# Performance work log

Hardware: AMD Instinct MI355X
Metric: run time of the kernel (lower is better)

The kernel has to match this reference:

```python
import jax, jax.numpy as jnp
import numpy as np

MOL_SIZE = 64      # points per molecule (all molecules equal-size -> block-diagonal attn)
NUM_HEADS = 8
CUTOFF = 8.0
NUM_RBF = 32
LN_EPS = 1e-5


def setup_inputs() -> dict:
    key = jax.random.key(0)
    ks = jax.random.split(key, 6)
    B, K, hidden = 1024, MOL_SIZE, 512
    H = NUM_HEADS
    N = B * K
    h = jax.random.normal(ks[0], (N, hidden), jnp.float32)
    pos = jax.random.normal(ks[1], (N, 3), jnp.float32) * 3.0  # spread so dists hit RBF centers
    batch = jnp.repeat(jnp.arange(B, dtype=jnp.int32), K)
    s = lambda fin: 1.0 / np.sqrt(fin)
    centers = jnp.linspace(0.0, CUTOFF, NUM_RBF).astype(jnp.float32)  # RBFEncoder buffer
    w_rbf = jax.random.normal(ks[2], (NUM_RBF, H), jnp.float32) * s(NUM_RBF)
    b_rbf = jnp.zeros((H,), jnp.float32)
    w_qkv = jax.random.normal(ks[3], (hidden, 3 * hidden), jnp.float32) * s(hidden)
    b_qkv = jnp.zeros((3 * hidden,), jnp.float32)
    w_out = jax.random.normal(ks[4], (hidden, hidden), jnp.float32) * s(hidden)
    b_out = jnp.zeros((hidden,), jnp.float32)
    gamma = jnp.ones((hidden,), jnp.float32)
    beta = jnp.zeros((hidden,), jnp.float32)
    return {"h": h, "pos": pos, "batch": batch, "centers": centers,
            "w_rbf": w_rbf, "b_rbf": b_rbf, "w_qkv": w_qkv, "b_qkv": b_qkv,
            "w_out": w_out, "b_out": b_out, "gamma": gamma, "beta": beta}


def reference(h, pos, batch, centers, w_rbf, b_rbf, w_qkv, b_qkv, w_out, b_out, gamma, beta):
    N, hidden = h.shape
    K = MOL_SIZE
    B = N // K
    H = NUM_HEADS
    D = hidden // H
    width = (CUTOFF / NUM_RBF) ** 2
    scale = D ** -0.5

    # equal-size contiguous molecules -> reshape equals per-molecule loop
    hb = h.reshape(B, K, hidden)
    pb = pos.reshape(B, K, 3)

    qkv = hb @ w_qkv + b_qkv                      # [B,K,3*hidden]
    q, k, v = jnp.split(qkv, 3, axis=-1)
    q = q.reshape(B, K, H, D)
    k = k.reshape(B, K, H, D)
    v = v.reshape(B, K, H, D)

    diff = pb[:, :, None, :] - pb[:, None, :, :]  # [B,K,K,3]
    dist = jnp.sqrt(jnp.maximum(jnp.sum(diff * diff, axis=-1), 1e-12))  # torch.cdist
    rbf = jnp.exp(-((dist[..., None] - centers) ** 2) / width)          # [B,K,K,R]
    bias = jnp.transpose(rbf @ w_rbf + b_rbf, (0, 3, 1, 2))             # [B,H,K,K]

    attn = jnp.einsum('bkhd,bjhd->bhkj', q, k) * scale + bias
    attn = jax.nn.softmax(attn, axis=-1)
    agg = jnp.einsum('bhkj,bjhd->bkhd', attn, v).reshape(B, K, hidden)
    out = agg @ w_out + b_out

    y = hb + out
    mu = jnp.mean(y, axis=-1, keepdims=True)
    var = jnp.var(y, axis=-1, keepdims=True)
    y = (y - mu) / jnp.sqrt(var + LN_EPS) * gamma + beta
    return y.reshape(N, hidden)
```

## Files before the change

### kernel.cpp

```cpp
#include <hip/hip_runtime.h>
#include <hip/hip_bf16.h>


#define HID 512
#define TBL 1024
#define DMAX 12.0f

typedef __attribute__((ext_vector_type(4))) float f32x4;
typedef __attribute__((ext_vector_type(8))) short bhalf8;

__device__ __forceinline__ short f2bf(float f) {
    union { float f; unsigned u; } x; x.f = f;
    unsigned u = x.u;
    unsigned r = (u + 0x7FFFu + ((u >> 16) & 1u)) >> 16;
    return (short)r;
}

__global__ __launch_bounds__(256) void k_prep_w(const float* __restrict__ w_qkv,
                                                const float* __restrict__ w_out,
                                                short* __restrict__ wqT,
                                                short* __restrict__ woT) {
    __shared__ short tile[64][68];
    const int t = threadIdx.x;
    int bt = blockIdx.x;
    const float* src; short* dst; int sld, tk, tc;
    if (bt < 192) { src = w_qkv; dst = wqT; sld = 1536; tk = bt & 7; tc = bt >> 3; }
    else { int b2 = bt - 192; src = w_out; dst = woT; sld = 512; tk = b2 & 7; tc = b2 >> 3; }
#pragma unroll
    for (int p = 0; p < 4; ++p) {
        int s = t + 256 * p;
        int r = s >> 4, sg = s & 15;
        const float4 v = *(const float4*)(src + (tk * 64 + r) * sld + tc * 64 + sg * 4);
        tile[r][sg * 4 + 0] = f2bf(v.x);
        tile[r][sg * 4 + 1] = f2bf(v.y);
        tile[r][sg * 4 + 2] = f2bf(v.z);
        tile[r][sg * 4 + 3] = f2bf(v.w);
    }
    __syncthreads();
#pragma unroll
    for (int p = 0; p < 16; ++p) {
        int o = t + 256 * p;
        int c = o >> 6, k = o & 63;
        dst[(tc * 64 + c) * 512 + tk * 64 + k] = tile[k][c];
    }
}

__global__ __launch_bounds__(256) void k_prep_tbl(const float* __restrict__ centers,
                                                  const float* __restrict__ w_rbf,
                                                  const float* __restrict__ b_rbf,
                                                  float* __restrict__ tbl) {
    int idx = blockIdx.x * 256 + threadIdx.x;
    int hh = idx >> 10, i = idx & (TBL - 1);
    float d = (float)i * (DMAX / (float)(TBL - 1));
    float s = b_rbf[hh];
    const float invw = 1.0f / 0.0625f;
#pragma unroll 4
    for (int r = 0; r < 32; ++r) {
        float tt = d - centers[r];
        s += w_rbf[r * 8 + hh] * expf(-(tt * tt) * invw);
    }
    tbl[idx] = s;
}

__global__ __launch_bounds__(512) void k_qkv(const float* __restrict__ h,
                                             const float* __restrict__ b_qkv,
                                             const short* __restrict__ wqT,
                                             short* __restrict__ qkvb,
                                             int molbase) {
    __shared__ __align__(16) short As[2][128 * 40];
    __shared__ __align__(16) short Bs[2][256 * 40];
    const int t = threadIdx.x;
    const int lane = t & 63, wave = t >> 6;
    const int l16 = lane & 15, g = lane >> 4;
    const int wrow = wave >> 2, wcol = wave & 3;
    const int R0 = molbase * 64 + blockIdx.x * 128;
    const int C0 = blockIdx.y * 256;

    f32x4 acc[4][4];
#pragma unroll
    for (int i = 0; i < 4; ++i)
#pragma unroll
        for (int j = 0; j < 4; ++j) acc[i][j] = (f32x4){0.f, 0.f, 0.f, 0.f};

    const int arow = t >> 2, aseg = t & 3;
    const float* hsrc = h + (size_t)(R0 + arow) * HID + aseg * 8;
    const int bcol = t >> 2, bseg = t & 3;
    const short* bsrc0 = wqT + (size_t)(C0 + bcol) * HID + bseg * 8;
    const short* bsrc1 = wqT + (size_t)(C0 + bcol + 128) * HID + bseg * 8;

    int4 pA, pB0, pB1;
#define QLOADA(kc) {                                                             \
        float4 a0 = *(const float4*)(hsrc + (kc) * 32);                          \
        float4 a1 = *(const float4*)(hsrc + (kc) * 32 + 4);                      \
        short s8[8];                                                             \
        s8[0] = f2bf(a0.x); s8[1] = f2bf(a0.y); s8[2] = f2bf(a0.z); s8[3] = f2bf(a0.w); \
        s8[4] = f2bf(a1.x); s8[5] = f2bf(a1.y); s8[6] = f2bf(a1.z); s8[7] = f2bf(a1.w); \
        pA = *(int4*)s8; }
#define QLOADB(kc) {                                                             \
        pB0 = *(const int4*)(bsrc0 + (kc) * 32);                                 \
        pB1 = *(const int4*)(bsrc1 + (kc) * 32); }
#define QSTAGE(buf) {                                                            \
        *(int4*)(&As[buf][arow * 40 + aseg * 8]) = pA;                           \
        *(int4*)(&Bs[buf][bcol * 40 + bseg * 8]) = pB0;                          \
        *(int4*)(&Bs[buf][(bcol + 128) * 40 + bseg * 8]) = pB1; }

    QLOADA(0); QLOADB(0); QSTAGE(0);
    __syncthreads();

    for (int kc = 0; kc < 16; ++kc) {
        const int cur = kc & 1;
        if (kc < 15) { QLOADA(kc + 1); QLOADB(kc + 1); }
        bhalf8 af[4], bf[4];
#pragma unroll
        for (int mt = 0; mt < 4; ++mt)
            af[mt] = *(const bhalf8*)(&As[cur][(wrow * 64 + mt * 16 + l16) * 40 + g * 8]);
#pragma unroll
        for (int nt = 0; nt < 4; ++nt)
            bf[nt] = *(const bhalf8*)(&Bs[cur][(wcol * 64 + nt * 16 + l16) * 40 + g * 8]);
#pragma unroll
        for (int mt = 0; mt < 4; ++mt)
#pragma unroll
            for (int nt = 0; nt < 4; ++nt)
                acc[mt][nt] = __builtin_amdgcn_mfma_f32_16x16x32_bf16(
                    af[mt], bf[nt], acc[mt][nt], 0, 0, 0);
        if (kc < 15) {
            QSTAGE(cur ^ 1);
            __syncthreads();
        }
    }
#undef QLOADA
#undef QLOADB
#undef QSTAGE

    const int sec = C0 >> 9;
    const float mul = (sec == 0) ? 0.125f : 1.0f;
#pragma unroll
    for (int nt = 0; nt < 4; ++nt) {
        int c = C0 + wcol * 64 + nt * 16 + l16;
        float bv = b_qkv[c];
        int head = (c >> 6) & 7, d = c & 63;
#pragma unroll
        for (int mt = 0; mt < 4; ++mt) {
            int rowg = R0 + wrow * 64 + mt * 16 + g * 4;
            int mol_local = (rowg >> 6) - molbase;
            int rloc = rowg & 63;
            short* panel = qkvb + (size_t)((mol_local * 3 + sec) * 8 + head) * 4096;
            if (sec == 2) {
#pragma unroll
                for (int r = 0; r < 4; ++r)
                    panel[d * 64 + rloc + r] = f2bf(acc[mt][nt][r] + bv);
            } else {
#pragma unroll
                for (int r = 0; r < 4; ++r)
                    panel[(rloc + r) * 64 + d] = f2bf((acc[mt][nt][r] + bv) * mul);
            }
        }
    }
}

__global__ __launch_bounds__(512) void k_fused(const short* __restrict__ qkvb,
                                               const float* __restrict__ pos,
                                               const float* __restrict__ tbl,
                                               const float* __restrict__ h,
                                               const short* __restrict__ woT,
                                               const float* __restrict__ b_out,
                                               const float* __restrict__ gamma,
                                               const float* __restrict__ beta,
                                               float* __restrict__ out,
                                               int molbase) {
    __shared__ __align__(16) short uP[8 * 4096];
    __shared__ float s_tbl[8 * 1032];
    __shared__ float s_px[64], s_py[64], s_pz[64];
    __shared__ float red[64 * 16];
    __shared__ float mr[64 * 2];

    const int t = threadIdx.x;
    const int wave = t >> 6, lane = t & 63;
    const int l16 = lane & 15, g = lane >> 4;
    const int mol_local = blockIdx.x;
    const int rowbase = (molbase + mol_local) * 64;

    for (int i = t; i < 8 * TBL; i += 512)
        s_tbl[(i >> 10) * 1032 + (i & (TBL - 1))] = tbl[i];
    if (t < 64) {
        s_px[t] = pos[(rowbase + t) * 3 + 0];
        s_py[t] = pos[(rowbase + t) * 3 + 1];
        s_pz[t] = pos[(rowbase + t) * 3 + 2];
    }
    __syncthreads();

    const short* qp = qkvb + ((size_t)(mol_local * 3 + 0) * 8 + wave) * 4096;
    const short* kp = qkvb + ((size_t)(mol_local * 3 + 1) * 8 + wave) * 4096;
    const short* vt = qkvb + ((size_t)(mol_local * 3 + 2) * 8 + wave) * 4096;

    f32x4 sacc[4][4];
#pragma unroll
    for (int i = 0; i < 4; ++i)
#pragma unroll
        for (int j = 0; j < 4; ++j) sacc[i][j] = (f32x4){0.f, 0.f, 0.f, 0.f};
#pragma unroll
    for (int kk = 0; kk < 2; ++kk) {
        bhalf8 qa[4], kb[4];
#pragma unroll
        for (int mt = 0; mt < 4; ++mt)
            qa[mt] = *(const bhalf8*)(qp + (mt * 16 + l16) * 64 + kk * 32 + g * 8);
#pragma unroll
        for (int nt = 0; nt < 4; ++nt)
            kb[nt] = *(const bhalf8*)(kp + (nt * 16 + l16) * 64 + kk * 32 + g * 8);
#pragma unroll
        for (int mt = 0; mt < 4; ++mt)
#pragma unroll
            for (int nt = 0; nt < 4; ++nt)
                sacc[mt][nt] = __builtin_amdgcn_mfma_f32_16x16x32_bf16(
                    qa[mt], kb[nt], sacc[mt][nt], 0, 0, 0);
    }

    const float tscale = (float)(TBL - 1) / DMAX;
    const float* T = s_tbl + wave * 1032;
#pragma unroll
    for (int nt = 0; nt < 4; ++nt) {
        int col = nt * 16 + l16;
        float cx = s_px[col], cy = s_py[col], cz = s_pz[col];
#pragma unroll
        for (int mt = 0; mt < 4; ++mt) {
#pragma unroll
            for (int r = 0; r < 4; ++r) {
                int row = mt * 16 + g * 4 + r;
                float dx = s_px[row] - cx, dy = s_py[row] - cy, dz = s_pz[row] - cz;
                float dd = fmaf(dx, dx, fmaf(dy, dy, dz * dz));
                float dist = sqrtf(fmaxf(dd, 1e-12f));
                float u = fminf(dist, DMAX) * tscale;
                int i = (int)u; if (i > TBL - 2) i = TBL - 2;
                float fr = u - (float)i;
                float t0 = T[i];
                sacc[mt][nt][r] += fmaf(fr, T[i + 1] - t0, t0);
            }
        }
    }

    float inv[4][4];
    short* Pw = uP + wave * 4096;
#pragma unroll
    for (int mt = 0; mt < 4; ++mt) {
#pragma unroll
        for (int r = 0; r < 4; ++r) {
            float m = fmaxf(fmaxf(sacc[mt][0][r], sacc[mt][1][r]),
                            fmaxf(sacc[mt][2][r], sacc[mt][3][r]));
#pragma unroll
            for (int off = 1; off < 16; off <<= 1) m = fmaxf(m, __shfl_xor(m, off, 64));
            float e[4], ssum = 0.f;
#pragma unroll
            for (int nt = 0; nt < 4; ++nt) { e[nt] = __expf(sacc[mt][nt][r] - m); ssum += e[nt]; }
#pragma unroll
            for (int off = 1; off < 16; off <<= 1) ssum += __shfl_xor(ssum, off, 64);
            inv[mt][r] = 1.0f / ssum;
            int row = mt * 16 + g * 4 + r;
            int rho = row & 7;
#pragma unroll
            for (int nt = 0; nt < 4; ++nt) {
                int c = nt * 16 + l16;
                Pw[row * 64 + (((c >> 3) ^ rho) << 3) + (c & 7)] = f2bf(e[nt]);
            }
        }
    }

    f32x4 oacc[4][4];
#pragma unroll
    for (int i = 0; i < 4; ++i)
#pragma unroll
        for (int j = 0; j < 4; ++j) oacc[i][j] = (f32x4){0.f, 0.f, 0.f, 0.f};
#pragma unroll
    for (int kk = 0; kk < 2; ++kk) {
        bhalf8 pa[4], vb[4];
#pragma unroll
        for (int mt = 0; mt < 4; ++mt)
            pa[mt] = *(const bhalf8*)(Pw + (mt * 16 + l16) * 64 +
                                      (((kk * 4 + g) ^ (l16 & 7)) << 3));
#pragma unroll
        for (int nt = 0; nt < 4; ++nt)
            vb[nt] = *(const bhalf8*)(vt + (nt * 16 + l16) * 64 + kk * 32 + g * 8);
#pragma unroll
        for (int mt = 0; mt < 4; ++mt)
#pragma unroll
            for (int nt = 0; nt < 4; ++nt)
                oacc[mt][nt] = __builtin_amdgcn_mfma_f32_16x16x32_bf16(
                    pa[mt], vb[nt], oacc[mt][nt], 0, 0, 0);
    }
#pragma unroll
    for (int mt = 0; mt < 4; ++mt)
#pragma unroll
        for (int nt = 0; nt < 4; ++nt)
#pragma unroll
            for (int r = 0; r < 4; ++r) oacc[mt][nt][r] *= inv[mt][r];

    __syncthreads();

#pragma unroll
    for (int mt = 0; mt < 4; ++mt) {
#pragma unroll
        for (int r = 0; r < 4; ++r) {
            int row = mt * 16 + g * 4 + r;
            int rho = row & 7;
#pragma unroll
            for (int nt = 0; nt < 4; ++nt) {
                int c = wave * 64 + nt * 16 + l16;
                uP[row * 512 + (((c >> 3) ^ rho) << 3) + (c & 7)] = f2bf(oacc[mt][nt][r]);
            }
        }
    }
    __syncthreads();

    f32x4 pacc[4][4];
#pragma unroll
    for (int i = 0; i < 4; ++i)
#pragma unroll
        for (int j = 0; j < 4; ++j) pacc[i][j] = (f32x4){0.f, 0.f, 0.f, 0.f};
#pragma unroll 4
    for (int kc = 0; kc < 16; ++kc) {
        bhalf8 af[4], bw[4];
#pragma unroll
        for (int mt = 0; mt < 4; ++mt)
            af[mt] = *(const bhalf8*)(uP + (mt * 16 + l16) * 512 +
                                      (((kc * 4 + g) ^ (l16 & 7)) << 3));
#pragma unroll
        for (int nt = 0; nt < 4; ++nt)
            bw[nt] = *(const bhalf8*)(woT + (size_t)(wave * 64 + nt * 16 + l16) * HID +
                                      kc * 32 + g * 8);
#pragma unroll
        for (int mt = 0; mt < 4; ++mt)
#pragma unroll
            for (int nt = 0; nt < 4; ++nt)
                pacc[mt][nt] = __builtin_amdgcn_mfma_f32_16x16x32_bf16(
                    af[mt], bw[nt], pacc[mt][nt], 0, 0, 0);
    }

#pragma unroll
    for (int mt = 0; mt < 4; ++mt) {
#pragma unroll
        for (int r = 0; r < 4; ++r) {
            int row = mt * 16 + g * 4 + r;
            float rs = 0.f, rq = 0.f;
#pragma unroll
            for (int nt = 0; nt < 4; ++nt) {
                int col = wave * 64 + nt * 16 + l16;
                float v = pacc[mt][nt][r] + b_out[col] +
                          h[(size_t)(rowbase + row) * HID + col];
                pacc[mt][nt][r] = v;
                rs += v;
                rq = fmaf(v, v, rq);
            }
#pragma unroll
            for (int off = 1; off < 16; off <<= 1) {
                rs += __shfl_xor(rs, off, 64);
                rq += __shfl_xor(rq, off, 64);
            }
            if (l16 == 0) {
                red[row * 16 + wave * 2 + 0] = rs;
                red[row * 16 + wave * 2 + 1] = rq;
            }
        }
    }
    __syncthreads();
    if (t < 64) {
        float s = 0.f, q = 0.f;
#pragma unroll
        for (int w = 0; w < 8; ++w) {
            s += red[t * 16 + w * 2 + 0];
            q += red[t * 16 + w * 2 + 1];
        }
        float mean = s * (1.0f / 512.0f);
        float var = q * (1.0f / 512.0f) - mean * mean;
        mr[t * 2 + 0] = mean;
        mr[t * 2 + 1] = rsqrtf(var + 1e-5f);
    }
    __syncthreads();
#pragma unroll
    for (int mt = 0; mt < 4; ++mt) {
#pragma unroll
        for (int r = 0; r < 4; ++r) {
            int row = mt * 16 + g * 4 + r;
            float mean = mr[row * 2 + 0], rstd = mr[row * 2 + 1];
#pragma unroll
            for (int nt = 0; nt < 4; ++nt) {
                int col = wave * 64 + nt * 16 + l16;
                out[(size_t)(rowbase + row) * HID + col] =
                    fmaf((pacc[mt][nt][r] - mean) * rstd, gamma[col], beta[col]);
            }
        }
    }
}

extern "C" void kernel_launch(void* const* d_in, const int* in_sizes, int n_in,
                              void* d_out, int out_size, void* d_ws, size_t ws_size,
                              hipStream_t stream) {
    (void)in_sizes; (void)n_in; (void)out_size; (void)ws_size;
    const float* h       = (const float*)d_in[0];
    const float* pos     = (const float*)d_in[1];
    const float* centers = (const float*)d_in[3];
    const float* w_rbf   = (const float*)d_in[4];
    const float* b_rbf   = (const float*)d_in[5];
    const float* w_qkv   = (const float*)d_in[6];
    const float* b_qkv   = (const float*)d_in[7];
    const float* w_out   = (const float*)d_in[8];
    const float* b_out   = (const float*)d_in[9];
    const float* gamma   = (const float*)d_in[10];
    const float* beta    = (const float*)d_in[11];
    float* out = (float*)d_out;

    char* ws = (char*)d_ws;
    short* wqT  = (short*)ws;
    short* woT  = (short*)(ws + 1572864);
    float* tbl  = (float*)(ws + 2097152);
    short* qkvb = (short*)(ws + 2162688);

    k_prep_w<<<256, 256, 0, stream>>>(w_qkv, w_out, wqT, woT);
    k_prep_tbl<<<32, 256, 0, stream>>>(centers, w_rbf, b_rbf, tbl);
    for (int half = 0; half < 2; ++half) {
        int molbase = half * 512;
        k_qkv<<<dim3(256, 6), 512, 0, stream>>>(h, b_qkv, wqT, qkvb, molbase);
        k_fused<<<512, 512, 0, stream>>>(qkvb, pos, tbl, h, woT, b_out,
                                         gamma, beta, out, molbase);
    }
}
```

Measured before the change: 420.6 us.

## Pre-convert h to bf16 and load QKV tiles via direct global-to-LDS with swizzle

Adds a separate pass that converts each half of h to swizzled bf16, and stores w_qkv transposed with an XOR swizzle. The QKV GEMM then uses global_load_lds to copy 64-wide K tiles straight into LDS, which removes register staging and the per-tile fp32 to bf16 conversion. It also remaps workgroups for L2 locality and vectorizes the V-panel stores. The trade-offs are an extra kernel launch and an extra round trip of h through memory per half, and the K loop loses its previous double buffering.

```diff
diff --git a/kernel.cpp b/kernel.cpp
--- a/kernel.cpp
+++ b/kernel.cpp
@@ -14,6 +14,11 @@
     unsigned u = x.u;
     unsigned r = (u + 0x7FFFu + ((u >> 16) & 1u)) >> 16;
     return (short)r;
+}
+
+__device__ __forceinline__ void gld_lds16(const void* g, void* l) {
+    __builtin_amdgcn_global_load_lds((const __attribute__((address_space(1))) void*)g,
+                                     (__attribute__((address_space(3))) void*)l, 16, 0, 0);
 }
 
 __global__ __launch_bounds__(256) void k_prep_w(const float* __restrict__ w_qkv,
@@ -23,9 +28,9 @@
     __shared__ short tile[64][68];
     const int t = threadIdx.x;
     int bt = blockIdx.x;
-    const float* src; short* dst; int sld, tk, tc;
-    if (bt < 192) { src = w_qkv; dst = wqT; sld = 1536; tk = bt & 7; tc = bt >> 3; }
-    else { int b2 = bt - 192; src = w_out; dst = woT; sld = 512; tk = b2 & 7; tc = b2 >> 3; }
+    const float* src; short* dst; int sld, tk, tc, swz;
+    if (bt < 192) { src = w_qkv; dst = wqT; sld = 1536; tk = bt & 7; tc = bt >> 3; swz = 1; }
+    else { int b2 = bt - 192; src = w_out; dst = woT; sld = 512; tk = b2 & 7; tc = b2 >> 3; swz = 0; }
 #pragma unroll
     for (int p = 0; p < 4; ++p) {
         int s = t + 256 * p;
@@ -41,7 +46,8 @@
     for (int p = 0; p < 16; ++p) {
         int o = t + 256 * p;
         int c = o >> 6, k = o & 63;
-        dst[(tc * 64 + c) * 512 + tk * 64 + k] = tile[k][c];
+        int kk = swz ? (k ^ ((c & 7) << 3)) : k;
+        dst[(tc * 64 + c) * 512 + tk * 64 + kk] = tile[k][c];
     }
 }
 
@@ -62,19 +68,37 @@
     tbl[idx] = s;
 }
 
-__global__ __launch_bounds__(512) void k_qkv(const float* __restrict__ h,
+__global__ __launch_bounds__(256) void k_prep_h(const float* __restrict__ h,
+                                                short* __restrict__ hbf,
+                                                int molbase) {
+    size_t i = ((size_t)blockIdx.x * 256 + threadIdx.x) * 8;
+    const float* src = h + (size_t)molbase * 64 * HID + i;
+    float4 a = *(const float4*)src;
+    float4 b = *(const float4*)(src + 4);
+    short s8[8];
+    s8[0] = f2bf(a.x); s8[1] = f2bf(a.y); s8[2] = f2bf(a.z); s8[3] = f2bf(a.w);
+    s8[4] = f2bf(b.x); s8[5] = f2bf(b.y); s8[6] = f2bf(b.z); s8[7] = f2bf(b.w);
+    int row = (int)(i >> 9);
+    size_t o = i ^ (size_t)((row & 7) << 3);
+    *(int4*)(hbf + o) = *(int4*)s8;
+}
+
+__global__ __launch_bounds__(512) void k_qkv(const short* __restrict__ hbf,
                                              const float* __restrict__ b_qkv,
                                              const short* __restrict__ wqT,
-                                             short* __restrict__ qkvb,
-                                             int molbase) {
-    __shared__ __align__(16) short As[2][128 * 40];
-    __shared__ __align__(16) short Bs[2][256 * 40];
+                                             short* __restrict__ qkvb) {
+    __shared__ __align__(16) short As[128 * 64];
+    __shared__ __align__(16) short Bs[256 * 64];
     const int t = threadIdx.x;
     const int lane = t & 63, wave = t >> 6;
     const int l16 = lane & 15, g = lane >> 4;
     const int wrow = wave >> 2, wcol = wave & 3;
-    const int R0 = molbase * 64 + blockIdx.x * 128;
-    const int C0 = blockIdx.y * 256;
+
+    int wg = blockIdx.x;
+    wg = (wg & 7) * 192 + (wg >> 3);
+    const int bx = wg & 255, by = wg >> 8;
+    const int R0l = bx * 128;
+    const int C0 = by * 256;
 
     f32x4 acc[4][4];
 #pragma unroll
@@ -82,55 +106,44 @@
 #pragma unroll
         for (int j = 0; j < 4; ++j) acc[i][j] = (f32x4){0.f, 0.f, 0.f, 0.f};
 
-    const int arow = t >> 2, aseg = t & 3;
-    const float* hsrc = h + (size_t)(R0 + arow) * HID + aseg * 8;
-    const int bcol = t >> 2, bseg = t & 3;
-    const short* bsrc0 = wqT + (size_t)(C0 + bcol) * HID + bseg * 8;
-    const short* bsrc1 = wqT + (size_t)(C0 + bcol + 128) * HID + bseg * 8;
-
-    int4 pA, pB0, pB1;
-#define QLOADA(kc) {                                                             \
-        float4 a0 = *(const float4*)(hsrc + (kc) * 32);                          \
-        float4 a1 = *(const float4*)(hsrc + (kc) * 32 + 4);                      \
-        short s8[8];                                                             \
-        s8[0] = f2bf(a0.x); s8[1] = f2bf(a0.y); s8[2] = f2bf(a0.z); s8[3] = f2bf(a0.w); \
-        s8[4] = f2bf(a1.x); s8[5] = f2bf(a1.y); s8[6] = f2bf(a1.z); s8[7] = f2bf(a1.w); \
-        pA = *(int4*)s8; }
-#define QLOADB(kc) {                                                             \
-        pB0 = *(const int4*)(bsrc0 + (kc) * 32);                                 \
-        pB1 = *(const int4*)(bsrc1 + (kc) * 32); }
-#define QSTAGE(buf) {                                                            \
-        *(int4*)(&As[buf][arow * 40 + aseg * 8]) = pA;                           \
-        *(int4*)(&Bs[buf][bcol * 40 + bseg * 8]) = pB0;                          \
-        *(int4*)(&Bs[buf][(bcol + 128) * 40 + bseg * 8]) = pB1; }
-
-    QLOADA(0); QLOADB(0); QSTAGE(0);
-    __syncthreads();
-
-    for (int kc = 0; kc < 16; ++kc) {
-        const int cur = kc & 1;
-        if (kc < 15) { QLOADA(kc + 1); QLOADB(kc + 1); }
-        bhalf8 af[4], bf[4];
-#pragma unroll
-        for (int mt = 0; mt < 4; ++mt)
-            af[mt] = *(const bhalf8*)(&As[cur][(wrow * 64 + mt * 16 + l16) * 40 + g * 8]);
-#pragma unroll
-        for (int nt = 0; nt < 4; ++nt)
-            bf[nt] = *(const bhalf8*)(&Bs[cur][(wcol * 64 + nt * 16 + l16) * 40 + g * 8]);
-#pragma unroll
-        for (int mt = 0; mt < 4; ++mt)
+    const int lrow = lane >> 3, lslot = lane & 7;
+    const int axor = (l16 & 7) << 3;
+
+    for (int kc = 0; kc < 8; ++kc) {
+        const int kb = kc * 64;
+#pragma unroll
+        for (int j = 0; j < 2; ++j) {
+            int row = wave * 16 + j * 8 + lrow;
+            gld_lds16(hbf + (size_t)(R0l + row) * HID + kb + lslot * 8,
+                      (char*)As + wave * 2048 + j * 1024 + lane * 16);
+        }
+#pragma unroll
+        for (int j = 0; j < 4; ++j) {
+            int row = wave * 32 + j * 8 + lrow;
+            gld_lds16(wqT + (size_t)(C0 + row) * HID + kb + lslot * 8,
+                      (char*)Bs + wave * 4096 + j * 1024 + lane * 16);
+        }
+        __syncthreads();
+#pragma unroll
+        for (int kk = 0; kk < 2; ++kk) {
+            const int c8 = kk * 32 + g * 8;
+            const int cs = c8 ^ axor;
+            bhalf8 af[4], bf[4];
+#pragma unroll
+            for (int mt = 0; mt < 4; ++mt)
+                af[mt] = *(const bhalf8*)(&As[(wrow * 64 + mt * 16 + l16) * 64 + cs]);
 #pragma unroll
             for (int nt = 0; nt < 4; ++nt)
-                acc[mt][nt] = __builtin_amdgcn_mfma_f32_16x16x32_bf16(
-                    af[mt], bf[nt], acc[mt][nt], 0, 0, 0);
-        if (kc < 15) {
-            QSTAGE(cur ^ 1);
-            __syncthreads();
-        }
-    }
-#undef QLOADA
-#undef QLOADB
-#undef QSTAGE
+                bf[nt] = *(const bhalf8*)(&Bs[(wcol * 64 + nt * 16 + l16) * 64 + cs]);
+#pragma unroll
+            for (int mt = 0; mt < 4; ++mt)
+#pragma unroll
+                for (int nt = 0; nt < 4; ++nt)
+                    acc[mt][nt] = __builtin_amdgcn_mfma_f32_16x16x32_bf16(
+                        af[mt], bf[nt], acc[mt][nt], 0, 0, 0);
+        }
+        __syncthreads();
+    }
 
     const int sec = C0 >> 9;
     const float mul = (sec == 0) ? 0.125f : 1.0f;
@@ -141,14 +154,17 @@
         int head = (c >> 6) & 7, d = c & 63;
 #pragma unroll
         for (int mt = 0; mt < 4; ++mt) {
-            int rowg = R0 + wrow * 64 + mt * 16 + g * 4;
-            int mol_local = (rowg >> 6) - molbase;
-            int rloc = rowg & 63;
+            int rowl = R0l + wrow * 64 + mt * 16 + g * 4;
+            int mol_local = rowl >> 6;
+            int rloc = rowl & 63;
             short* panel = qkvb + (size_t)((mol_local * 3 + sec) * 8 + head) * 4096;
             if (sec == 2) {
-#pragma unroll
-                for (int r = 0; r < 4; ++r)
-                    panel[d * 64 + rloc + r] = f2bf(acc[mt][nt][r] + bv);
+                short4 s4;
+                s4.x = f2bf(acc[mt][nt][0] + bv);
+                s4.y = f2bf(acc[mt][nt][1] + bv);
+                s4.z = f2bf(acc[mt][nt][2] + bv);
+                s4.w = f2bf(acc[mt][nt][3] + bv);
+                *(short4*)(panel + d * 64 + rloc) = s4;
             } else {
 #pragma unroll
                 for (int r = 0; r < 4; ++r)
@@ -411,13 +427,15 @@
     short* wqT  = (short*)ws;
     short* woT  = (short*)(ws + 1572864);
     float* tbl  = (float*)(ws + 2097152);
-    short* qkvb = (short*)(ws + 2162688);
+    short* hbf  = (short*)(ws + 2162688);
+    short* qkvb = (short*)(ws + 35717120);
 
     k_prep_w<<<256, 256, 0, stream>>>(w_qkv, w_out, wqT, woT);
     k_prep_tbl<<<32, 256, 0, stream>>>(centers, w_rbf, b_rbf, tbl);
     for (int half = 0; half < 2; ++half) {
         int molbase = half * 512;
-        k_qkv<<<dim3(256, 6), 512, 0, stream>>>(h, b_qkv, wqT, qkvb, molbase);
+        k_prep_h<<<8192, 256, 0, stream>>>(h, hbf, molbase);
+        k_qkv<<<1536, 512, 0, stream>>>(hbf, b_qkv, wqT, qkvb);
         k_fused<<<512, 512, 0, stream>>>(qkvb, pos, tbl, h, woT, b_out,
                                          gamma, beta, out, molbase);
     }
```

Result: faster. 408.7 us (-2.8%).
